# Optimization experiments

Measured on AMD Instinct MI355X. Metric: run time of the kernel, lower is better.

## Reference

```python
import jax, jax.numpy as jnp
import numpy as np

B, D, T, H, K = 16, 1024, 1024, 1024, 2  # batch, in_channels, seq_len, hidden_size, kernel_size


def setup_inputs() -> dict:
    key = jax.random.key(0)
    k1, k2, k3 = jax.random.split(key, 3)
    inputs = jax.random.normal(k1, (B, D, T), dtype=jnp.float32)
    # Conv1D kernel in OIH layout: [3H, D, K]; scaled to keep gates in a sane range
    conv_w = jax.random.normal(k2, (3 * H, D, K), dtype=jnp.float32) / np.float32(np.sqrt(D * K))
    conv_b = jax.random.normal(k3, (3 * H,), dtype=jnp.float32) * 0.01
    return {"inputs": inputs, "conv_w": conv_w, "conv_b": conv_b}


def reference(inputs, conv_w, conv_b):
    # inputs: [B, D, T] (channels_first, as in the keras call signature)
    # Causal conv: left-pad time by K-1, then VALID conv -> [B, 3H, T]
    padded = jnp.pad(inputs, ((0, 0), (0, 0), (K - 1, 0)))
    gates = jax.lax.conv_general_dilated(
        padded, conv_w, window_strides=(1,), padding="VALID",
        dimension_numbers=("NCH", "OIH", "NCH"))
    gates = gates + conv_b[None, :, None]
    gates = jnp.transpose(gates, (0, 2, 1))  # [B, T, 3H]
    z = jnp.tanh(gates[..., :H])
    f = jax.nn.sigmoid(gates[..., H:2 * H])
    o = jax.nn.sigmoid(gates[..., 2 * H:])

    # fo-pooling linear recurrence: c_t = f_t * c_{t-1} + (1 - f_t) * z_t, c_0 = 0
    zf = (jnp.transpose(z, (1, 0, 2)), jnp.transpose(f, (1, 0, 2)))  # time-major [T, B, H]

    def step(c, zf_t):
        z_t, f_t = zf_t
        c_new = f_t * c + (1.0 - f_t) * z_t
        return c_new, c_new

    c0 = jnp.zeros((B, H), dtype=inputs.dtype)
    _, c_seq = jax.lax.scan(step, c0, zf)
    c_seq = jnp.transpose(c_seq, (1, 0, 2))  # [B, T, H]
    h_seq = o * c_seq
    return c_seq, h_seq
```

## Files before the change

### kernel.cpp

```cpp
#include <hip/hip_runtime.h>

#define Bsz 16
#define Dch 1024
#define Tsz 1024
#define Hsz 1024
#define Mtot (Bsz*Tsz)
#define K2   (2*Dch)
#define Ntot (3*Hsz)
#define NCH  16
#define CL   64

typedef __attribute__((ext_vector_type(8))) short bf16x8;
typedef __attribute__((ext_vector_type(4))) float f32x4;

__device__ __forceinline__ unsigned short f2bf(float x) {
    unsigned u = __float_as_uint(x);
    u += 0x7FFFu + ((u >> 16) & 1u);
    return (unsigned short)(u >> 16);
}
__device__ __forceinline__ float bf2f(unsigned short s) {
    return __uint_as_float(((unsigned)s) << 16);
}

#define GLOAD_LDS16(gp, lp) \
    __builtin_amdgcn_global_load_lds((const __attribute__((address_space(1))) void*)(gp), \
                                     (__attribute__((address_space(3))) void*)(lp), 16, 0, 0)

__global__ void prep_w(const float* __restrict__ w, unsigned short* __restrict__ wb) {
    int i = blockIdx.x * blockDim.x + threadIdx.x;
    float4 v = ((const float4*)w)[i];
    ushort4 r;
    r.x = f2bf(v.x); r.y = f2bf(v.y); r.z = f2bf(v.z); r.w = f2bf(v.w);
    ((ushort4*)wb)[i] = r;
}

__global__ void prep_a(const float* __restrict__ x, unsigned short* __restrict__ a2) {
    __shared__ float Xs[64][66];
    int bid = blockIdx.x;
    int b   = bid >> 8;
    int tt0 = ((bid >> 4) & 15) << 6;
    int dd0 = (bid & 15) << 6;
    int tid  = threadIdx.x;
    int colt = tid & 63, rowq = tid >> 6;
    const size_t xbase = (size_t)b * (Dch * Tsz);
    #pragma unroll
    for (int r = 0; r < 16; r++) {
        int dd = r * 4 + rowq;
        Xs[dd][1 + colt] = x[xbase + (size_t)(dd0 + dd) * Tsz + tt0 + colt];
    }
    if (tid < 64) {
        Xs[tid][0] = (tt0 == 0) ? 0.f : x[xbase + (size_t)(dd0 + tid) * Tsz + tt0 - 1];
    }
    __syncthreads();
    #pragma unroll
    for (int r = 0; r < 16; r++) {
        int tr = r * 4 + rowq;
        int dc = colt;
        float v0 = Xs[dc][tr];
        float v1 = Xs[dc][tr + 1];
        unsigned pack = (unsigned)f2bf(v0) | ((unsigned)f2bf(v1) << 16);
        int m = (b << 10) + tt0 + tr;
        ((unsigned*)a2)[(size_t)m * (K2 / 2) + dd0 + dc] = pack;
    }
}

__global__ __launch_bounds__(256)
void gemm_gates(const unsigned short* __restrict__ A, const unsigned short* __restrict__ Bt,
                const float* __restrict__ bias,
                float* __restrict__ zc, float* __restrict__ fh, unsigned short* __restrict__ ob) {
    __shared__ __align__(16) unsigned short As[128 * 64];
    __shared__ __align__(16) unsigned short Bs2[128 * 64];
    int tid = threadIdx.x;
    int n0 = blockIdx.x << 7;
    int m0 = blockIdx.y << 7;
    int wave = tid >> 6, lane = tid & 63;
    int wm = wave & 1, wn = wave >> 1;
    int lm = lane & 15, q = lane >> 4;

    int lrow = lane >> 3, lchunk = lane & 7;
    int gch  = lchunk ^ lrow;
    const unsigned short* Ag = A  + (size_t)(m0 + wave * 32 + lrow) * K2 + gch * 8;
    const unsigned short* Bg = Bt + (size_t)(n0 + wave * 32 + lrow) * K2 + gch * 8;

    f32x4 acc[4][4] = {};
    for (int kb = 0; kb < K2; kb += 64) {
        #pragma unroll
        for (int j = 0; j < 4; j++) {
            int rbase = wave * 32 + j * 8;
            GLOAD_LDS16(Ag + (size_t)j * 8 * K2 + kb, &As[rbase * 64]);
            GLOAD_LDS16(Bg + (size_t)j * 8 * K2 + kb, &Bs2[rbase * 64]);
        }
        __syncthreads();
        #pragma unroll
        for (int ks = 0; ks < 64; ks += 32) {
            bf16x8 af[4], bfr[4];
            int cs = ks >> 3;
            int sw = (lm & 7);
            #pragma unroll
            for (int i = 0; i < 4; i++)
                af[i] = *(bf16x8*)&As[(wm * 64 + i * 16 + lm) * 64 + (((cs + q) ^ sw) << 3)];
            #pragma unroll
            for (int j = 0; j < 4; j++)
                bfr[j] = *(bf16x8*)&Bs2[(wn * 64 + j * 16 + lm) * 64 + (((cs + q) ^ sw) << 3)];
            #pragma unroll
            for (int i = 0; i < 4; i++)
                #pragma unroll
                for (int j = 0; j < 4; j++)
                    acc[i][j] = __builtin_amdgcn_mfma_f32_16x16x32_bf16(af[i], bfr[j], acc[i][j], 0, 0, 0);
        }
        __syncthreads();
    }
    int gt = n0 >> 10;
    #pragma unroll
    for (int i = 0; i < 4; i++) {
        int mrow = m0 + wm * 64 + i * 16 + q * 4;
        #pragma unroll
        for (int j = 0; j < 4; j++) {
            int n = n0 + wn * 64 + j * 16 + lm;
            float bv = bias[n];
            int hcol = n & 1023;
            #pragma unroll
            for (int r = 0; r < 4; r++) {
                float g = acc[i][j][r] + bv;
                size_t idx = (size_t)(mrow + r) * Hsz + hcol;
                if (gt == 0) {
                    float e = __expf(2.f * g);
                    zc[idx] = __fdividef(e - 1.f, e + 1.f);
                } else {
                    float s = __fdividef(1.f, 1.f + __expf(-g));
                    if (gt == 1) fh[idx] = s;
                    else         ob[idx] = f2bf(s);
                }
            }
        }
    }
}

__global__ __launch_bounds__(256)
void scan1(const float* __restrict__ zc, const float* __restrict__ fh,
           float* __restrict__ Aw, float* __restrict__ Bw) {
    int blk = blockIdx.x;
    int hb = blk & 3, ch = (blk >> 2) & 15, b = blk >> 6;
    int h = hb * 256 + threadIdx.x;
    size_t base = ((size_t)b << 20) + ((size_t)(ch * CL) << 10) + h;
    float a = 1.f, bb = 0.f;
    #pragma unroll 8
    for (int s = 0; s < CL; s++) {
        size_t idx = base + ((size_t)s << 10);
        float z = zc[idx], f = fh[idx];
        a *= f;
        bb = z + f * (bb - z);
    }
    int o = (ch * Bsz + b) * Hsz + h;
    Aw[o] = a; Bw[o] = bb;
}

__global__ __launch_bounds__(256)
void scan2(const float* __restrict__ Aw, const float* __restrict__ Bw,
           float* __restrict__ C0) {
    int g = blockIdx.x * 256 + threadIdx.x;
    int b = g >> 10, h = g & 1023;
    float c = 0.f;
    #pragma unroll
    for (int ch = 0; ch < NCH; ch++) {
        int o = (ch * Bsz + b) * Hsz + h;
        C0[o] = c;
        c = Aw[o] * c + Bw[o];
    }
}

__global__ __launch_bounds__(256)
void scan3(float* __restrict__ zc, float* __restrict__ fh,
           const unsigned short* __restrict__ ob, const float* __restrict__ C0) {
    int blk = blockIdx.x;
    int hb = blk & 3, ch = (blk >> 2) & 15, b = blk >> 6;
    int h = hb * 256 + threadIdx.x;
    size_t base = ((size_t)b << 20) + ((size_t)(ch * CL) << 10) + h;
    float c = C0[(ch * Bsz + b) * Hsz + h];
    #pragma unroll 8
    for (int s = 0; s < CL; s++) {
        size_t idx = base + ((size_t)s << 10);
        float z = zc[idx];
        float f = fh[idx];
        float o = bf2f(ob[idx]);
        c = z + f * (c - z);
        zc[idx] = c;
        fh[idx] = o * c;
    }
}

extern "C" void kernel_launch(void* const* d_in, const int* in_sizes, int n_in,
                              void* d_out, int out_size, void* d_ws, size_t ws_size,
                              hipStream_t stream) {
    const float* x    = (const float*)d_in[0];
    const float* w    = (const float*)d_in[1];
    const float* bias = (const float*)d_in[2];
    float* zc = (float*)d_out;
    float* fh = (float*)d_out + (size_t)Mtot * Hsz;
    unsigned short* a2 = (unsigned short*)d_ws;
    unsigned short* wb = a2 + (size_t)Mtot * K2;
    unsigned short* ob = wb + (size_t)Ntot * K2;
    float* Aw = (float*)(ob + (size_t)Mtot * Hsz);
    float* Bw = Aw + NCH * Bsz * Hsz;
    float* C0 = Bw + NCH * Bsz * Hsz;

    hipLaunchKernelGGL(prep_w, dim3(6144), dim3(256), 0, stream, w, wb);
    hipLaunchKernelGGL(prep_a, dim3(4096), dim3(256), 0, stream, x, a2);
    hipLaunchKernelGGL(gemm_gates, dim3(24, 128), dim3(256), 0, stream, a2, wb, bias, zc, fh, ob);
    hipLaunchKernelGGL(scan1, dim3(1024), dim3(256), 0, stream, zc, fh, Aw, Bw);
    hipLaunchKernelGGL(scan2, dim3(64), dim3(256), 0, stream, Aw, Bw, C0);
    hipLaunchKernelGGL(scan3, dim3(1024), dim3(256), 0, stream, zc, fh, ob, C0);
}
```

Baseline: 517.6 us.

## Merge prep kernels, fold carry-scan into scan3, vectorize scans by two

```diff
diff --git a/kernel.cpp b/kernel.cpp
--- a/kernel.cpp
+++ b/kernel.cpp
@@ -26,21 +26,27 @@
     __builtin_amdgcn_global_load_lds((const __attribute__((address_space(1))) void*)(gp), \
                                      (__attribute__((address_space(3))) void*)(lp), 16, 0, 0)
 
-__global__ void prep_w(const float* __restrict__ w, unsigned short* __restrict__ wb) {
-    int i = blockIdx.x * blockDim.x + threadIdx.x;
-    float4 v = ((const float4*)w)[i];
-    ushort4 r;
-    r.x = f2bf(v.x); r.y = f2bf(v.y); r.z = f2bf(v.z); r.w = f2bf(v.w);
-    ((ushort4*)wb)[i] = r;
-}
-
-__global__ void prep_a(const float* __restrict__ x, unsigned short* __restrict__ a2) {
+__global__ __launch_bounds__(256)
+void prep(const float* __restrict__ x, unsigned short* __restrict__ a2,
+          const float* __restrict__ w, unsigned short* __restrict__ wb) {
     __shared__ float Xs[64][66];
     int bid = blockIdx.x;
+    int tid = threadIdx.x;
+    if (bid >= 4096) {
+        int i0 = (bid - 4096) * 256 + tid;
+        #pragma unroll
+        for (int k = 0; k < 4; k++) {
+            int i = i0 + k * (1536 * 256);
+            float4 v = ((const float4*)w)[i];
+            ushort4 r;
+            r.x = f2bf(v.x); r.y = f2bf(v.y); r.z = f2bf(v.z); r.w = f2bf(v.w);
+            ((ushort4*)wb)[i] = r;
+        }
+        return;
+    }
     int b   = bid >> 8;
     int tt0 = ((bid >> 4) & 15) << 6;
     int dd0 = (bid & 15) << 6;
-    int tid  = threadIdx.x;
     int colt = tid & 63, rowq = tid >> 6;
     const size_t xbase = (size_t)b * (Dch * Tsz);
     #pragma unroll
@@ -140,52 +146,52 @@
 void scan1(const float* __restrict__ zc, const float* __restrict__ fh,
            float* __restrict__ Aw, float* __restrict__ Bw) {
     int blk = blockIdx.x;
-    int hb = blk & 3, ch = (blk >> 2) & 15, b = blk >> 6;
-    int h = hb * 256 + threadIdx.x;
+    int hb = blk & 1, ch = (blk >> 1) & 15, b = blk >> 5;
+    int h = hb * 512 + threadIdx.x * 2;
     size_t base = ((size_t)b << 20) + ((size_t)(ch * CL) << 10) + h;
-    float a = 1.f, bb = 0.f;
+    float ax = 1.f, ay = 1.f, bx = 0.f, by = 0.f;
     #pragma unroll 8
     for (int s = 0; s < CL; s++) {
         size_t idx = base + ((size_t)s << 10);
-        float z = zc[idx], f = fh[idx];
-        a *= f;
-        bb = z + f * (bb - z);
+        float2 z = *(const float2*)&zc[idx];
+        float2 f = *(const float2*)&fh[idx];
+        ax *= f.x; ay *= f.y;
+        bx = z.x + f.x * (bx - z.x);
+        by = z.y + f.y * (by - z.y);
     }
     int o = (ch * Bsz + b) * Hsz + h;
-    Aw[o] = a; Bw[o] = bb;
-}
-
-__global__ __launch_bounds__(256)
-void scan2(const float* __restrict__ Aw, const float* __restrict__ Bw,
-           float* __restrict__ C0) {
-    int g = blockIdx.x * 256 + threadIdx.x;
-    int b = g >> 10, h = g & 1023;
-    float c = 0.f;
-    #pragma unroll
-    for (int ch = 0; ch < NCH; ch++) {
-        int o = (ch * Bsz + b) * Hsz + h;
-        C0[o] = c;
-        c = Aw[o] * c + Bw[o];
-    }
+    *(float2*)&Aw[o] = make_float2(ax, ay);
+    *(float2*)&Bw[o] = make_float2(bx, by);
 }
 
 __global__ __launch_bounds__(256)
 void scan3(float* __restrict__ zc, float* __restrict__ fh,
-           const unsigned short* __restrict__ ob, const float* __restrict__ C0) {
+           const unsigned short* __restrict__ ob,
+           const float* __restrict__ Aw, const float* __restrict__ Bw) {
     int blk = blockIdx.x;
-    int hb = blk & 3, ch = (blk >> 2) & 15, b = blk >> 6;
-    int h = hb * 256 + threadIdx.x;
+    int hb = blk & 1, ch = (blk >> 1) & 15, b = blk >> 5;
+    int h = hb * 512 + threadIdx.x * 2;
+    float cx = 0.f, cy = 0.f;
+    for (int cp = 0; cp < ch; cp++) {
+        int o = (cp * Bsz + b) * Hsz + h;
+        float2 A = *(const float2*)&Aw[o];
+        float2 B = *(const float2*)&Bw[o];
+        cx = A.x * cx + B.x;
+        cy = A.y * cy + B.y;
+    }
     size_t base = ((size_t)b << 20) + ((size_t)(ch * CL) << 10) + h;
-    float c = C0[(ch * Bsz + b) * Hsz + h];
     #pragma unroll 8
     for (int s = 0; s < CL; s++) {
         size_t idx = base + ((size_t)s << 10);
-        float z = zc[idx];
-        float f = fh[idx];
-        float o = bf2f(ob[idx]);
-        c = z + f * (c - z);
-        zc[idx] = c;
-        fh[idx] = o * c;
+        float2 z = *(const float2*)&zc[idx];
+        float2 f = *(const float2*)&fh[idx];
+        unsigned ov = *(const unsigned*)&ob[idx];
+        cx = z.x + f.x * (cx - z.x);
+        cy = z.y + f.y * (cy - z.y);
+        *(float2*)&zc[idx] = make_float2(cx, cy);
+        float ox = bf2f((unsigned short)(ov & 0xFFFF));
+        float oy = bf2f((unsigned short)(ov >> 16));
+        *(float2*)&fh[idx] = make_float2(ox * cx, oy * cy);
     }
 }
 
@@ -202,12 +208,9 @@
     unsigned short* ob = wb + (size_t)Ntot * K2;
     float* Aw = (float*)(ob + (size_t)Mtot * Hsz);
     float* Bw = Aw + NCH * Bsz * Hsz;
-    float* C0 = Bw + NCH * Bsz * Hsz;
-
-    hipLaunchKernelGGL(prep_w, dim3(6144), dim3(256), 0, stream, w, wb);
-    hipLaunchKernelGGL(prep_a, dim3(4096), dim3(256), 0, stream, x, a2);
+
+    hipLaunchKernelGGL(prep, dim3(5632), dim3(256), 0, stream, x, a2, w, wb);
     hipLaunchKernelGGL(gemm_gates, dim3(24, 128), dim3(256), 0, stream, a2, wb, bias, zc, fh, ob);
-    hipLaunchKernelGGL(scan1, dim3(1024), dim3(256), 0, stream, zc, fh, Aw, Bw);
-    hipLaunchKernelGGL(scan2, dim3(64), dim3(256), 0, stream, Aw, Bw, C0);
-    hipLaunchKernelGGL(scan3, dim3(1024), dim3(256), 0, stream, zc, fh, ob, C0);
-}
+    hipLaunchKernelGGL(scan1, dim3(512), dim3(256), 0, stream, zc, fh, Aw, Bw);
+    hipLaunchKernelGGL(scan3, dim3(512), dim3(256), 0, stream, zc, fh, ob, Aw, Bw);
+}
```

After: 510.7 us. About the same (-1.3%).
